# Optimization experiments

Hardware: AMD Instinct MI355X
Metric: run time of the kernel (lower is better)

The kernel has to match this reference:

```python
import jax, jax.numpy as jnp
import numpy as np

B = 262144
C = 128
NUM_CLASSES = 128   # fill_max for y
PAD = 2048
EPS = 1e-8
REJECT_THRESHOLD = 1


def setup_inputs() -> dict:
    key = jax.random.key(0)
    kx, ky = jax.random.split(key)
    x = jax.random.normal(kx, (B, C), dtype=jnp.float32)
    y = jax.random.randint(ky, (B,), 0, NUM_CLASSES)
    return {"x": x, "y": y}


def _decorrelate_loss(x, y):
    Bn, Cn = x.shape
    # per-class counts / sums (segment reduce replaces the python loop + boolean mask)
    counts = jax.ops.segment_sum(jnp.ones((Bn,), x.dtype), y, num_segments=NUM_CLASSES)  # [K]
    counts_i = counts.astype(jnp.int32)
    sums = jax.ops.segment_sum(x, y, num_segments=NUM_CLASSES)                            # [K, C]
    mean = sums / jnp.maximum(counts, 1.0)[:, None]
    centered = x - mean[y]                                                                # [B, C]
    # unbiased variance per class (torch .var default), guarded for count<=1
    var = jax.ops.segment_sum(centered * centered, y, num_segments=NUM_CLASSES) \
        / jnp.maximum(counts - 1.0, 1.0)[:, None]                                         # [K, C]
    xn = centered / jnp.sqrt(EPS + var)[y]                                                # [B, C]
    # sort rows by class so each class occupies a contiguous block, then slice fixed-size
    order = jnp.argsort(y)
    xs = jnp.concatenate([xn[order], jnp.zeros((PAD, Cn), x.dtype)], axis=0)              # [B+PAD, C]
    cum = jnp.cumsum(counts_i)
    starts = jnp.concatenate([jnp.zeros((1,), jnp.int32), cum[:-1]])                      # exclusive cumsum
    gathered = jax.vmap(lambda s: jax.lax.dynamic_slice(xs, (s, 0), (PAD, Cn)))(starts)   # [K, PAD, C]
    row_valid = (jnp.arange(PAD)[None, :] < counts_i[:, None]).astype(x.dtype)            # [K, PAD]
    g = gathered * row_valid[:, :, None]
    # per-class correlation matrices, all at once
    corr = jnp.einsum('kpc,kpd->kcd', g, g)                                               # [K, C, C]
    sq_sum = jnp.sum(corr * corr, axis=(1, 2))                                            # [K]
    diag_sq = jnp.sum(jnp.einsum('kcc->kc', corr) ** 2, axis=1)                           # [K]
    off_mean = (sq_sum - diag_sq) / (Cn * (Cn - 1))                                       # off_diagonal(.)^2 mean
    valid = counts_i > REJECT_THRESHOLD
    loss = jnp.sum(jnp.where(valid, off_mean, 0.0))
    n_count = jnp.sum(jnp.where(valid, counts, 0.0))
    return jnp.where(n_count > 0, loss / n_count, 0.0)


def reference(x, y):
    return _decorrelate_loss(x, y)
```

## Files before the change

### kernel.cpp

```cpp
#include <hip/hip_runtime.h>

#define B_ROWS   262144
#define C_DIM    128
#define K_CLS    128
#define PAD_R    2048
#define PAD2     4096
#define QSPLIT   4
#define QROWS    (PAD_R / QSPLIT)
#define TROWS    32
#define LSTRIDE  132
#define EPS_F    1e-8f
#define CHUNK    1024
#define G_CHUNKS 256

typedef float f32x4  __attribute__((ext_vector_type(4)));
typedef short bf16x8 __attribute__((ext_vector_type(8)));

__device__ __forceinline__ unsigned f2bf(float f) {
  unsigned u = __float_as_uint(f);
  return (u + 0x7fffu + ((u >> 16) & 1u)) >> 16;
}
__device__ __forceinline__ unsigned packbf(float a, float b) {
  return f2bf(a) | (f2bf(b) << 16);
}

#define TILE_BARRIER()                                      \
  do {                                                      \
    asm volatile("s_waitcnt lgkmcnt(0)" ::: "memory");      \
    __builtin_amdgcn_s_barrier();                           \
  } while (0)

__global__ __launch_bounds__(256) void hist_kernel(const int* __restrict__ y,
                                                   int* __restrict__ hist,
                                                   float* __restrict__ numden) {
  __shared__ int h[K_CLS];
  int g = blockIdx.x, tid = threadIdx.x;
  if (g == 0 && tid < 64) numden[tid] = 0.f;
  if (tid < K_CLS) h[tid] = 0;
  __syncthreads();
  for (int j = tid; j < CHUNK; j += 256) atomicAdd(&h[y[g * CHUNK + j]], 1);
  __syncthreads();
  if (tid < K_CLS) hist[g * K_CLS + tid] = h[tid];
}

__global__ __launch_bounds__(256) void scan_kernel(int* __restrict__ hist,
                                                   int* __restrict__ counts) {
  __shared__ int s[G_CHUNKS];
  int k = blockIdx.x, g = threadIdx.x;
  int v = hist[g * K_CLS + k];
  s[g] = v;
  __syncthreads();
  for (int off = 1; off < G_CHUNKS; off <<= 1) {
    int t = (g >= off) ? s[g - off] : 0;
    __syncthreads();
    s[g] += t;
    __syncthreads();
  }
  hist[g * K_CLS + k] = s[g] - v;
  if (g == G_CHUNKS - 1) counts[k] = s[g];
}

__global__ __launch_bounds__(256) void rank_kernel(const int* __restrict__ y,
                                                   const int* __restrict__ hist,
                                                   int* __restrict__ ord) {
  __shared__ unsigned short cnt_sub[16][K_CLS];
  __shared__ int offs[K_CLS];
  const int g = blockIdx.x, tid = threadIdx.x;
  const int lane = tid & 63, w = tid >> 6;
  if (tid < K_CLS) offs[tid] = hist[g * K_CLS + tid];
  {
    unsigned int* cz = (unsigned int*)cnt_sub;
    for (int i = tid; i < 16 * K_CLS / 2; i += 256) cz[i] = 0;
  }
  __syncthreads();

  int yv[4], rig[4];
  #pragma unroll
  for (int i = 0; i < 4; ++i) {
    const int s = w * 4 + i;
    const int yy = y[g * CHUNK + s * 64 + lane];
    unsigned long long m = ~0ULL;
    #pragma unroll
    for (int b = 0; b < 7; ++b) {
      unsigned long long bb = __ballot((yy >> b) & 1);
      m &= ((yy >> b) & 1) ? bb : ~bb;
    }
    const unsigned long long lt = (1ULL << lane) - 1ULL;
    rig[i] = (int)__popcll(m & lt);
    yv[i] = yy;
    const int leader = __ffsll((long long)m) - 1;
    if (lane == leader) cnt_sub[s][yy] = (unsigned short)__popcll(m);
  }
  __syncthreads();

  if (tid < K_CLS) {
    int run = 0;
    #pragma unroll
    for (int s = 0; s < 16; ++s) {
      int t = cnt_sub[s][tid];
      cnt_sub[s][tid] = (unsigned short)run;
      run += t;
    }
  }
  __syncthreads();

  #pragma unroll
  for (int i = 0; i < 4; ++i) {
    const int s = w * 4 + i;
    const int k = yv[i];
    const int R = offs[k] + (int)cnt_sub[s][k] + rig[i];
    if (R < PAD2) ord[k * PAD2 + R] = g * CHUNK + s * 64 + lane;
  }
}

__global__ __launch_bounds__(512, 4) void gemm_kernel(const float* __restrict__ x,
                                                      const int* __restrict__ ord,
                                                      const int* __restrict__ counts,
                                                      float* __restrict__ spart,
                                                      float* __restrict__ sums_part,
                                                      float* __restrict__ sqs_part,
                                                      float* __restrict__ ovfs_part) {
  __shared__ unsigned int lds[2 * (TROWS / 2) * LSTRIDE];
  __shared__ int ord_l[QROWS];
  const int blk = blockIdx.x;
  const int k = blk >> 2, quarter = blk & 3;
  const int cnt_full = counts[k];
  const int T = cnt_full < PAD_R ? cnt_full : PAD_R;
  const int r_base = quarter * QROWS;
  const int rend = (T < r_base + QROWS) ? T : (r_base + QROWS);
  const int nr = rend - r_base;
  const int nt = (nr > 0) ? ((nr + TROWS - 1) / TROWS) : 0;

  const int tid = threadIdx.x;
  const int lane = tid & 63;
  const int w = tid >> 6;
  const int wr = w >> 1, wc = w & 1;
  const int p = tid >> 5;
  const int lc = tid & 31;

  f32x4 acc[2][4];
  #pragma unroll
  for (int i = 0; i < 2; ++i)
    #pragma unroll
    for (int j = 0; j < 4; ++j) acc[i][j] = (f32x4){0.f, 0.f, 0.f, 0.f};
  float sum4[4] = {0.f, 0.f, 0.f, 0.f}, sq4[4] = {0.f, 0.f, 0.f, 0.f};

  const int* ordk = ord + k * PAD2;

  if (tid < QROWS) {
    int vi = ordk[r_base + tid];
    ord_l[tid] = ((unsigned)vi < B_ROWS) ? vi : 0;
  }
  __syncthreads();

  auto load_tile = [&](int t, f32x4* vv) {
    const int rr = t * TROWS + 2 * p;
    const int2 idx = *(const int2*)(&ord_l[rr]);
    const size_t co = (size_t)(lc << 2);
    vv[0] = *(const f32x4*)(x + (size_t)idx.x * C_DIM + co);
    vv[1] = *(const f32x4*)(x + (size_t)idx.y * C_DIM + co);
  };

  auto write_tile = [&](unsigned int* buf, const f32x4* vv, int t) {
    const int rg = r_base + t * TROWS + 2 * p;
    const f32x4 z = (f32x4){0.f, 0.f, 0.f, 0.f};
    const f32x4 w0 = (rg + 0 < rend) ? vv[0] : z;
    const f32x4 w1 = (rg + 1 < rend) ? vv[1] : z;
    #pragma unroll
    for (int e = 0; e < 4; ++e) {
      sum4[e] += w0[e] + w1[e];
      sq4[e] += w0[e] * w0[e] + w1[e] * w1[e];
    }
    uint4 pk;
    pk.x = packbf(w0[0], w1[0]);
    pk.y = packbf(w0[1], w1[1]);
    pk.z = packbf(w0[2], w1[2]);
    pk.w = packbf(w0[3], w1[3]);
    *(uint4*)(&buf[p * LSTRIDE + (lc << 2)]) = pk;
  };

  auto compute_tile = [&](const unsigned int* buf) {
    const int q2 = lane >> 4;
    const int fr = lane & 15;
    const unsigned int* base = buf + q2 * 4 * LSTRIDE;
    bf16x8 afr[2], bfr[4];
    #pragma unroll
    for (int mi = 0; mi < 2; ++mi) {
      const int c = wr * 32 + mi * 16 + fr;
      union { int4 i; bf16x8 h; } u;
      u.i.x = base[0 * LSTRIDE + c];
      u.i.y = base[1 * LSTRIDE + c];
      u.i.z = base[2 * LSTRIDE + c];
      u.i.w = base[3 * LSTRIDE + c];
      afr[mi] = u.h;
    }
    #pragma unroll
    for (int ni = 0; ni < 4; ++ni) {
      const int d = wc * 64 + ni * 16 + fr;
      union { int4 i; bf16x8 h; } u;
      u.i.x = base[0 * LSTRIDE + d];
      u.i.y = base[1 * LSTRIDE + d];
      u.i.z = base[2 * LSTRIDE + d];
      u.i.w = base[3 * LSTRIDE + d];
      bfr[ni] = u.h;
    }
    #pragma unroll
    for (int mi = 0; mi < 2; ++mi)
      #pragma unroll
      for (int ni = 0; ni < 4; ++ni)
        acc[mi][ni] = __builtin_amdgcn_mfma_f32_16x16x32_bf16(afr[mi], bfr[ni], acc[mi][ni], 0, 0, 0);
  };

  const int BUFSZ = (TROWS / 2) * LSTRIDE;
  if (nt > 0) {
    f32x4 vA[2], vB[2];
    load_tile(0, vA);
    if (nt > 1) load_tile(1, vB);
    write_tile(lds, vA, 0);
    if (nt > 2) load_tile(2, vA);
    TILE_BARRIER();
    int cur = 0;
    for (int t = 0; t < nt; t += 2) {
      if (t + 1 < nt) {
        write_tile(lds + (unsigned)(cur ^ 1) * BUFSZ, vB, t + 1);
        if (t + 3 < nt) load_tile(t + 3, vB);
      }
      compute_tile(lds + (unsigned)cur * BUFSZ);
      TILE_BARRIER();
      cur ^= 1;
      if (t + 1 >= nt) break;
      if (t + 2 < nt) {
        write_tile(lds + (unsigned)(cur ^ 1) * BUFSZ, vA, t + 2);
        if (t + 4 < nt) load_tile(t + 4, vA);
      }
      compute_tile(lds + (unsigned)cur * BUFSZ);
      TILE_BARRIER();
      cur ^= 1;
    }
  }

  float osum[4] = {0.f, 0.f, 0.f, 0.f}, osq[4] = {0.f, 0.f, 0.f, 0.f};
  const int colo = lc << 2;
  for (int r = PAD_R + quarter + (p << 2); r < cnt_full; r += 64) {
    int row = ordk[r];
    f32x4 vv = *(const f32x4*)(x + (size_t)row * C_DIM + colo);
    #pragma unroll
    for (int e = 0; e < 4; ++e) { float t = vv[e]; osum[e] += t; osq[e] += t * t; }
  }

  __syncthreads();
  float* red = (float*)lds;
  if (tid < 3 * C_DIM) red[tid] = 0.f;
  __syncthreads();
  #pragma unroll
  for (int e = 0; e < 4; ++e) {
    atomicAdd(&red[colo + e], sum4[e]);
    atomicAdd(&red[C_DIM + colo + e], sq4[e] + osq[e]);
    atomicAdd(&red[2 * C_DIM + colo + e], osum[e]);
  }
  __syncthreads();
  if (tid < C_DIM) {
    sums_part[(quarter * K_CLS + k) * C_DIM + tid] = red[tid];
    sqs_part [(quarter * K_CLS + k) * C_DIM + tid] = red[C_DIM + tid];
    ovfs_part[(quarter * K_CLS + k) * C_DIM + tid] = red[2 * C_DIM + tid];
  }
  float* sp = spart + (size_t)(quarter * K_CLS + k) * (C_DIM * C_DIM);
  #pragma unroll
  for (int mi = 0; mi < 2; ++mi)
    #pragma unroll
    for (int ni = 0; ni < 4; ++ni)
      #pragma unroll
      for (int r = 0; r < 4; ++r) {
        int c = wr * 32 + mi * 16 + ((lane >> 4) << 2) + r;
        int d = wc * 64 + ni * 16 + (lane & 15);
        sp[c * C_DIM + d] = acc[mi][ni][r];
      }
}

__global__ __launch_bounds__(512) void finalize_kernel(const float* __restrict__ spart,
                                                       const float* __restrict__ sums_part,
                                                       const float* __restrict__ sqs_part,
                                                       const float* __restrict__ ovfs_part,
                                                       const int* __restrict__ counts,
                                                       float* __restrict__ numden) {
  __shared__ float m_l[C_DIM], is_l[C_DIM], st_l[C_DIM];
  __shared__ float wred[8];
  int k = blockIdx.x, tid = threadIdx.x;
  int count = counts[k];
  float Tf = (float)(count < PAD_R ? count : PAD_R);
  if (tid < C_DIM) {
    float s_tr = 0.f, osum = 0.f, fsq = 0.f;
    #pragma unroll
    for (int j = 0; j < QSPLIT; ++j) {
      s_tr += sums_part[(j * K_CLS + k) * C_DIM + tid];
      osum += ovfs_part[(j * K_CLS + k) * C_DIM + tid];
      fsq  += sqs_part [(j * K_CLS + k) * C_DIM + tid];
    }
    float fsum = s_tr + osum;
    float cf = (float)count;
    float m = fsum / fmaxf(cf, 1.f);
    float var = (fsq - cf * m * m) / fmaxf(cf - 1.f, 1.f);
    m_l[tid] = m;
    is_l[tid] = rsqrtf(var + EPS_F);
    st_l[tid] = s_tr;
  }
  __syncthreads();
  float local = 0.f;
  for (int e4 = tid * 4; e4 < C_DIM * C_DIM; e4 += 512 * 4) {
    int c = e4 >> 7, d0 = e4 & 127;
    f32x4 sa = (f32x4){0.f, 0.f, 0.f, 0.f};
    #pragma unroll
    for (int j = 0; j < QSPLIT; ++j) {
      f32x4 sj = *(const f32x4*)(spart + (size_t)(j * K_CLS + k) * (C_DIM * C_DIM) + e4);
      #pragma unroll
      for (int e = 0; e < 4; ++e) sa[e] += sj[e];
    }
    #pragma unroll
    for (int e = 0; e < 4; ++e) {
      int d = d0 + e;
      float corr = is_l[c] * is_l[d] *
                   (sa[e] - m_l[c] * st_l[d] - m_l[d] * st_l[c] + Tf * m_l[c] * m_l[d]);
      if (c != d) local += corr * corr;
    }
  }
  for (int off = 32; off > 0; off >>= 1) local += __shfl_down(local, off);
  int lane = tid & 63, wid = tid >> 6;
  if (lane == 0) wred[wid] = local;
  __syncthreads();
  if (tid == 0 && count > 1) {
    float tot = 0.f;
    #pragma unroll
    for (int i = 0; i < 8; ++i) tot += wred[i];
    atomicAdd(&numden[0], tot * (1.f / (float)(C_DIM * (C_DIM - 1))));
    atomicAdd(&numden[1], (float)count);
  }
}

__global__ void div_kernel(const float* __restrict__ numden, float* __restrict__ out) {
  if (threadIdx.x == 0 && blockIdx.x == 0)
    out[0] = numden[1] > 0.f ? numden[0] / numden[1] : 0.f;
}

extern "C" void kernel_launch(void* const* d_in, const int* in_sizes, int n_in,
                              void* d_out, int out_size, void* d_ws, size_t ws_size,
                              hipStream_t stream) {
  (void)in_sizes; (void)n_in; (void)out_size; (void)ws_size;
  const float* x = (const float*)d_in[0];
  const int*   y = (const int*)d_in[1];
  float* out = (float*)d_out;
  char* ws = (char*)d_ws;

  float* numden    = (float*)(ws + 0);
  int*   hist      = (int*)(ws + 256);
  int*   counts    = (int*)(ws + 131328);
  int*   ord       = (int*)(ws + 132096);
  float* sums_part = (float*)(ws + 2229248);
  float* sqs_part  = (float*)(ws + 2491392);
  float* ovfs_part = (float*)(ws + 2753536);
  float* spart     = (float*)(ws + 3015680);

  hist_kernel<<<G_CHUNKS, 256, 0, stream>>>(y, hist, numden);
  scan_kernel<<<K_CLS, 256, 0, stream>>>(hist, counts);
  rank_kernel<<<G_CHUNKS, 256, 0, stream>>>(y, hist, ord);
  gemm_kernel<<<QSPLIT * K_CLS, 512, 0, stream>>>(x, ord, counts, spart, sums_part,
                                                  sqs_part, ovfs_part);
  finalize_kernel<<<K_CLS, 512, 0, stream>>>(spart, sums_part, sqs_part, ovfs_part,
                                             counts, numden);
  div_kernel<<<1, 64, 0, stream>>>(numden, out);
}
```

Measured before the change: 71.12 us.

## Use 32x32x16 MFMA with swizzled LDS layout, 64-row tiles, split finalize

The gemm kernel now stages 64-row tiles in a column-major, XOR-swizzled LDS layout so each lane fetches a contiguous bf16x8 fragment, and it issues 32x32x16 bf16 MFMAs instead of 16x16x32. This cuts the number of LDS reads and MFMA instructions per tile and halves the barrier count per row. Separately, the finalize kernel is split four ways per class to raise parallelism in the epilogue, with only one split adding the count. The trade-offs are more register pressure from 16-wide accumulators and four loaded rows per thread, and redundant per-column stat computation across the four finalize blocks.

```diff
diff --git a/kernel.cpp b/kernel.cpp
--- a/kernel.cpp
+++ b/kernel.cpp
@@ -7,13 +7,14 @@
 #define PAD2     4096
 #define QSPLIT   4
 #define QROWS    (PAD_R / QSPLIT)
-#define TROWS    32
-#define LSTRIDE  132
+#define FSPLIT   4
+#define TROWS    64
 #define EPS_F    1e-8f
 #define CHUNK    1024
 #define G_CHUNKS 256
 
 typedef float f32x4  __attribute__((ext_vector_type(4)));
+typedef float f32x16 __attribute__((ext_vector_type(16)));
 typedef short bf16x8 __attribute__((ext_vector_type(8)));
 
 __device__ __forceinline__ unsigned f2bf(float f) {
@@ -22,6 +23,10 @@
 }
 __device__ __forceinline__ unsigned packbf(float a, float b) {
   return f2bf(a) | (f2bf(b) << 16);
+}
+__device__ __forceinline__ int swz(int c) { return ((c >> 2) ^ c) & 7; }
+__device__ __forceinline__ int lidx(int c, int kp) {
+  return c * 32 + ((((kp >> 2) ^ swz(c)) << 2) | (kp & 3));
 }
 
 #define TILE_BARRIER()                                      \
@@ -120,7 +125,7 @@
                                                       float* __restrict__ sums_part,
                                                       float* __restrict__ sqs_part,
                                                       float* __restrict__ ovfs_part) {
-  __shared__ unsigned int lds[2 * (TROWS / 2) * LSTRIDE];
+  __shared__ unsigned int lds[2 * C_DIM * 32];
   __shared__ int ord_l[QROWS];
   const int blk = blockIdx.x;
   const int k = blk >> 2, quarter = blk & 3;
@@ -134,86 +139,77 @@
   const int tid = threadIdx.x;
   const int lane = tid & 63;
   const int w = tid >> 6;
-  const int wr = w >> 1, wc = w & 1;
+  const int qr = w >> 1, qc = w & 1;
   const int p = tid >> 5;
   const int lc = tid & 31;
 
-  f32x4 acc[2][4];
+  f32x16 acc[2];
   #pragma unroll
   for (int i = 0; i < 2; ++i)
     #pragma unroll
-    for (int j = 0; j < 4; ++j) acc[i][j] = (f32x4){0.f, 0.f, 0.f, 0.f};
+    for (int j = 0; j < 16; ++j) acc[i][j] = 0.f;
   float sum4[4] = {0.f, 0.f, 0.f, 0.f}, sq4[4] = {0.f, 0.f, 0.f, 0.f};
 
   const int* ordk = ord + k * PAD2;
 
-  if (tid < QROWS) {
+  {
     int vi = ordk[r_base + tid];
     ord_l[tid] = ((unsigned)vi < B_ROWS) ? vi : 0;
   }
   __syncthreads();
 
   auto load_tile = [&](int t, f32x4* vv) {
-    const int rr = t * TROWS + 2 * p;
-    const int2 idx = *(const int2*)(&ord_l[rr]);
+    const int rr = t * TROWS + 4 * p;
+    const int4 idx = *(const int4*)(&ord_l[rr]);
     const size_t co = (size_t)(lc << 2);
     vv[0] = *(const f32x4*)(x + (size_t)idx.x * C_DIM + co);
     vv[1] = *(const f32x4*)(x + (size_t)idx.y * C_DIM + co);
+    vv[2] = *(const f32x4*)(x + (size_t)idx.z * C_DIM + co);
+    vv[3] = *(const f32x4*)(x + (size_t)idx.w * C_DIM + co);
   };
 
   auto write_tile = [&](unsigned int* buf, const f32x4* vv, int t) {
-    const int rg = r_base + t * TROWS + 2 * p;
+    const int rg = r_base + t * TROWS + 4 * p;
     const f32x4 z = (f32x4){0.f, 0.f, 0.f, 0.f};
     const f32x4 w0 = (rg + 0 < rend) ? vv[0] : z;
     const f32x4 w1 = (rg + 1 < rend) ? vv[1] : z;
+    const f32x4 w2 = (rg + 2 < rend) ? vv[2] : z;
+    const f32x4 w3 = (rg + 3 < rend) ? vv[3] : z;
     #pragma unroll
     for (int e = 0; e < 4; ++e) {
-      sum4[e] += w0[e] + w1[e];
-      sq4[e] += w0[e] * w0[e] + w1[e] * w1[e];
-    }
-    uint4 pk;
-    pk.x = packbf(w0[0], w1[0]);
-    pk.y = packbf(w0[1], w1[1]);
-    pk.z = packbf(w0[2], w1[2]);
-    pk.w = packbf(w0[3], w1[3]);
-    *(uint4*)(&buf[p * LSTRIDE + (lc << 2)]) = pk;
+      sum4[e] += (w0[e] + w1[e]) + (w2[e] + w3[e]);
+      sq4[e] += (w0[e] * w0[e] + w1[e] * w1[e]) + (w2[e] * w2[e] + w3[e] * w3[e]);
+    }
+    #pragma unroll
+    for (int e = 0; e < 4; ++e) {
+      const int c = (lc << 2) + e;
+      uint2 pk;
+      pk.x = packbf(w0[e], w1[e]);
+      pk.y = packbf(w2[e], w3[e]);
+      *(uint2*)(&buf[lidx(c, 2 * p)]) = pk;
+    }
   };
 
   auto compute_tile = [&](const unsigned int* buf) {
-    const int q2 = lane >> 4;
-    const int fr = lane & 15;
-    const unsigned int* base = buf + q2 * 4 * LSTRIDE;
-    bf16x8 afr[2], bfr[4];
-    #pragma unroll
-    for (int mi = 0; mi < 2; ++mi) {
-      const int c = wr * 32 + mi * 16 + fr;
-      union { int4 i; bf16x8 h; } u;
-      u.i.x = base[0 * LSTRIDE + c];
-      u.i.y = base[1 * LSTRIDE + c];
-      u.i.z = base[2 * LSTRIDE + c];
-      u.i.w = base[3 * LSTRIDE + c];
-      afr[mi] = u.h;
-    }
-    #pragma unroll
-    for (int ni = 0; ni < 4; ++ni) {
-      const int d = wc * 64 + ni * 16 + fr;
-      union { int4 i; bf16x8 h; } u;
-      u.i.x = base[0 * LSTRIDE + d];
-      u.i.y = base[1 * LSTRIDE + d];
-      u.i.z = base[2 * LSTRIDE + d];
-      u.i.w = base[3 * LSTRIDE + d];
-      bfr[ni] = u.h;
-    }
-    #pragma unroll
-    for (int mi = 0; mi < 2; ++mi)
+    const int h = lane >> 5;
+    const int r32 = lane & 31;
+    #pragma unroll
+    for (int s = 0; s < 4; ++s) {
+      const int kp0 = 8 * s + 4 * h;
+      const int cA = qr * 32 + r32;
+      bf16x8 a = *(const bf16x8*)(&buf[lidx(cA, kp0)]);
       #pragma unroll
-      for (int ni = 0; ni < 4; ++ni)
-        acc[mi][ni] = __builtin_amdgcn_mfma_f32_16x16x32_bf16(afr[mi], bfr[ni], acc[mi][ni], 0, 0, 0);
+      for (int ni = 0; ni < 2; ++ni) {
+        const int dB = qc * 64 + ni * 32 + r32;
+        bf16x8 b = *(const bf16x8*)(&buf[lidx(dB, kp0)]);
+        acc[ni] = __builtin_amdgcn_mfma_f32_32x32x16_bf16(a, b, acc[ni], 0, 0, 0);
+      }
+    }
   };
 
-  const int BUFSZ = (TROWS / 2) * LSTRIDE;
+  const int BUFSZ = C_DIM * 32;
   if (nt > 0) {
-    f32x4 vA[2], vB[2];
+    f32x4 vA[4], vB[4];
     load_tile(0, vA);
     if (nt > 1) load_tile(1, vB);
     write_tile(lds, vA, 0);
@@ -265,16 +261,17 @@
     ovfs_part[(quarter * K_CLS + k) * C_DIM + tid] = red[2 * C_DIM + tid];
   }
   float* sp = spart + (size_t)(quarter * K_CLS + k) * (C_DIM * C_DIM);
-  #pragma unroll
-  for (int mi = 0; mi < 2; ++mi)
-    #pragma unroll
-    for (int ni = 0; ni < 4; ++ni)
+  {
+    const int h = lane >> 5, r32 = lane & 31;
+    #pragma unroll
+    for (int ni = 0; ni < 2; ++ni)
       #pragma unroll
-      for (int r = 0; r < 4; ++r) {
-        int c = wr * 32 + mi * 16 + ((lane >> 4) << 2) + r;
-        int d = wc * 64 + ni * 16 + (lane & 15);
-        sp[c * C_DIM + d] = acc[mi][ni][r];
+      for (int r = 0; r < 16; ++r) {
+        int c = qr * 32 + (r & 3) + 8 * (r >> 2) + 4 * h;
+        int d = qc * 64 + ni * 32 + r32;
+        sp[c * C_DIM + d] = acc[ni][r];
       }
+  }
 }
 
 __global__ __launch_bounds__(512) void finalize_kernel(const float* __restrict__ spart,
@@ -285,9 +282,10 @@
                                                        float* __restrict__ numden) {
   __shared__ float m_l[C_DIM], is_l[C_DIM], st_l[C_DIM];
   __shared__ float wred[8];
-  int k = blockIdx.x, tid = threadIdx.x;
-  int count = counts[k];
-  float Tf = (float)(count < PAD_R ? count : PAD_R);
+  const int k = blockIdx.x >> 2, fs = blockIdx.x & 3;
+  const int tid = threadIdx.x;
+  const int count = counts[k];
+  const float Tf = (float)(count < PAD_R ? count : PAD_R);
   if (tid < C_DIM) {
     float s_tr = 0.f, osum = 0.f, fsq = 0.f;
     #pragma unroll
@@ -306,7 +304,9 @@
   }
   __syncthreads();
   float local = 0.f;
-  for (int e4 = tid * 4; e4 < C_DIM * C_DIM; e4 += 512 * 4) {
+  const int e_lo = fs * (C_DIM * C_DIM / FSPLIT);
+  const int e_hi = e_lo + (C_DIM * C_DIM / FSPLIT);
+  for (int e4 = e_lo + tid * 4; e4 < e_hi; e4 += 512 * 4) {
     int c = e4 >> 7, d0 = e4 & 127;
     f32x4 sa = (f32x4){0.f, 0.f, 0.f, 0.f};
     #pragma unroll
@@ -332,7 +332,7 @@
     #pragma unroll
     for (int i = 0; i < 8; ++i) tot += wred[i];
     atomicAdd(&numden[0], tot * (1.f / (float)(C_DIM * (C_DIM - 1))));
-    atomicAdd(&numden[1], (float)count);
+    if (fs == 0) atomicAdd(&numden[1], (float)count);
   }
 }
 
@@ -364,7 +364,7 @@
   rank_kernel<<<G_CHUNKS, 256, 0, stream>>>(y, hist, ord);
   gemm_kernel<<<QSPLIT * K_CLS, 512, 0, stream>>>(x, ord, counts, spart, sums_part,
                                                   sqs_part, ovfs_part);
-  finalize_kernel<<<K_CLS, 512, 0, stream>>>(spart, sums_part, sqs_part, ovfs_part,
-                                             counts, numden);
+  finalize_kernel<<<FSPLIT * K_CLS, 512, 0, stream>>>(spart, sums_part, sqs_part,
+                                                      ovfs_part, counts, numden);
   div_kernel<<<1, 64, 0, stream>>>(numden, out);
 }
```

Measured after the change: 83.20 us. 1.17x slower.
